# Kernel tuning notes

Measured on AMD Instinct MI355X. Metric: run time of the kernel, lower is better.

## Reference

```python
import jax, jax.numpy as jnp
import numpy as np

B, S, D, F, E, K, T = 4, 2048, 1024, 4096, 8, 2, 64


def setup_inputs() -> dict:
    key = jax.random.key(0)
    ks = jax.random.split(key, 12)
    s = 0.02
    return {
        "inputs": jax.random.normal(ks[0], (B, S, D), jnp.float32),
        "task_param": jax.random.normal(ks[1], (B, S, T), jnp.float32),
        "alpha": jnp.array(0.5, jnp.float32),
        "Wg_in": jax.random.normal(ks[2], (D, E), jnp.float32) * s,
        "bg_in": jnp.zeros((E,), jnp.float32),
        "Wg_task": jax.random.normal(ks[3], (T, E), jnp.float32) * s,
        "bg_task": jnp.zeros((E,), jnp.float32),
        "W1": jax.random.normal(ks[4], (E, D, F), jnp.float32) * s,
        "b1": jnp.zeros((E, F), jnp.float32),
        "W2": jax.random.normal(ks[5], (E, F, D), jnp.float32) * s,
        "b2": jnp.zeros((E, D), jnp.float32),
    }


def reference(inputs, task_param, alpha, Wg_in, bg_in, Wg_task, bg_task, W1, b1, W2, b2):
    dtype = inputs.dtype
    # blended gate logits: (1-alpha)*input_gate(x) + alpha*task_gate(task)
    gate_logits = (1.0 - alpha) * (jnp.einsum("bsd,de->bse", inputs, Wg_in) + bg_in) \
                + alpha * (jnp.einsum("bst,te->bse", task_param, Wg_task) + bg_task)
    # top-k expert selection (torch.topk: sorted descending)
    topk_vals, selected = jax.lax.top_k(gate_logits, K)  # [B,S,K]
    # aux load-balancing loss
    weights_softmax = jax.nn.softmax(gate_logits.astype(jnp.float32), axis=-1).astype(dtype)
    average_weight = weights_softmax.mean(axis=(0, 1))                 # [E]
    onehot = jax.nn.one_hot(selected, E, dtype=jnp.float32)            # [B,S,K,E]
    average_count = onehot.sum(axis=2).mean(axis=(0, 1)).astype(dtype) # [E]
    l_aux = jnp.mean(average_weight * average_count) * E
    # combine weights: softmax over the K selected logits, scattered to expert slots
    w = jax.nn.softmax(topk_vals.astype(jnp.float32), axis=-1).astype(dtype)  # [B,S,K]
    combine = jnp.einsum("bsk,bske->bse", w.astype(jnp.float32), onehot).astype(dtype)  # [B,S,E]
    # dense dispatch/combine (math-equivalent to boolean-mask gather/scatter loop)
    results = jnp.zeros_like(inputs)
    for e in range(E):
        h = jax.nn.gelu(jnp.einsum("bsd,df->bsf", inputs, W1[e]) + b1[e])
        y = jnp.einsum("bsf,fd->bsd", h, W2[e]) + b2[e]
        results = results + combine[..., e:e + 1] * y
    return (results, l_aux.astype(jnp.float32))
```

## Files before the change

### kernel.cpp

```cpp
#include <hip/hip_runtime.h>

#define NTOK 8192
#define DDIM 1024
#define FDIM 4096
#define NEXP 8
#define TDIM 64
#define MAXBLK 72

#define H_OFF   (1u<<20)
#define W1B_OFF (H_OFF + 134217728u)
#define W2B_OFF (W1B_OFF + 67108864u)
#define XB_OFF  (W2B_OFF + 67108864u)
#define FULL_WS (XB_OFF + 16777216u)

typedef __bf16 bf16x8 __attribute__((ext_vector_type(8)));
typedef unsigned short u16x8 __attribute__((ext_vector_type(8)));
typedef unsigned short u16x4 __attribute__((ext_vector_type(4)));
typedef float f32x4 __attribute__((ext_vector_type(4)));

__device__ __forceinline__ float gelu_tanh(float h) {
  float u = 0.7978845608028654f * (h + 0.044715f * h * h * h);
  float e = __expf(2.0f * u);
  return 0.5f * h * (2.0f - 2.0f / (e + 1.0f));
}

__device__ __forceinline__ void glds16(const void* g, void* l) {
  __builtin_amdgcn_global_load_lds((const __attribute__((address_space(1))) void*)g,
                                   (__attribute__((address_space(3))) void*)l, 16, 0, 0);
}

#define VM8() asm volatile("s_waitcnt vmcnt(8)" ::: "memory")
#define VM4() asm volatile("s_waitcnt vmcnt(4)" ::: "memory")
#define VM0() asm volatile("s_waitcnt vmcnt(0)" ::: "memory")
#define BAR() __builtin_amdgcn_s_barrier()

__global__ __launch_bounds__(256) void gate_kernel(
    const float* __restrict__ x, const float* __restrict__ task,
    const float* __restrict__ alpha_p,
    const float* __restrict__ Wg_in, const float* __restrict__ bg_in,
    const float* __restrict__ Wg_task, const float* __restrict__ bg_task,
    int* __restrict__ cnt, float* __restrict__ wsum,
    int* __restrict__ tok_list, float* __restrict__ wt_list)
{
  __shared__ float s_wsum[NEXP];
  int tid = threadIdx.x;
  if (tid < NEXP) s_wsum[tid] = 0.0f;
  __syncthreads();

  int lane = tid & 63;
  int wid  = tid >> 6;
  int tok  = blockIdx.x * 4 + wid;
  float a  = alpha_p[0];

  const float* xr = x + (size_t)tok * DDIM;
  float accd[8] = {0,0,0,0,0,0,0,0};
#pragma unroll
  for (int i = 0; i < DDIM/64; ++i) {
    int d = lane + 64*i;
    float xv = xr[d];
    f32x4 wa = *(const f32x4*)(Wg_in + (size_t)d*8);
    f32x4 wb = *(const f32x4*)(Wg_in + (size_t)d*8 + 4);
#pragma unroll
    for (int j = 0; j < 4; ++j) {
      accd[j]   = fmaf(xv, wa[j], accd[j]);
      accd[4+j] = fmaf(xv, wb[j], accd[4+j]);
    }
  }
  float part[8];
  {
    int d = lane;
    float tv = task[(size_t)tok*TDIM + d];
    f32x4 wa = *(const f32x4*)(Wg_task + (size_t)d*8);
    f32x4 wb = *(const f32x4*)(Wg_task + (size_t)d*8 + 4);
#pragma unroll
    for (int j = 0; j < 4; ++j) {
      part[j]   = (1.0f-a)*accd[j]   + a*(tv*wa[j]);
      part[4+j] = (1.0f-a)*accd[4+j] + a*(tv*wb[j]);
    }
  }
#pragma unroll
  for (int e = 0; e < 8; ++e) {
#pragma unroll
    for (int m = 1; m < 64; m <<= 1) part[e] += __shfl_xor(part[e], m);
  }

  if (lane == 0) {
    float lg[8];
#pragma unroll
    for (int e = 0; e < 8; ++e) lg[e] = part[e] + (1.0f-a)*bg_in[e] + a*bg_task[e];
    int e0 = 0;
#pragma unroll
    for (int e = 1; e < 8; ++e) if (lg[e] > lg[e0]) e0 = e;
    int e1 = (e0 == 0) ? 1 : 0;
#pragma unroll
    for (int e = 0; e < 8; ++e) if (e != e0 && lg[e] > lg[e1]) e1 = e;
    float mx = lg[0];
#pragma unroll
    for (int e = 1; e < 8; ++e) mx = fmaxf(mx, lg[e]);
    float p[8], s = 0.0f;
#pragma unroll
    for (int e = 0; e < 8; ++e) { p[e] = __expf(lg[e] - mx); s += p[e]; }
    float inv = 1.0f / s;
#pragma unroll
    for (int e = 0; e < 8; ++e) atomicAdd(&s_wsum[e], p[e] * inv);
    float p1 = __expf(lg[e1] - lg[e0]);
    float w0 = 1.0f / (1.0f + p1);
    float w1 = p1 * w0;
    int pos0 = atomicAdd(&cnt[e0], 1);
    tok_list[e0*NTOK + pos0] = tok; wt_list[e0*NTOK + pos0] = w0;
    int pos1 = atomicAdd(&cnt[e1], 1);
    tok_list[e1*NTOK + pos1] = tok; wt_list[e1*NTOK + pos1] = w1;
  }
  __syncthreads();
  if (tid < NEXP) atomicAdd(&wsum[tid], s_wsum[tid]);
}

__global__ void finalize_kernel(const int* __restrict__ cnt, const float* __restrict__ wsum,
                                int* __restrict__ offs, float* __restrict__ laux,
                                int* __restrict__ blk_e, int* __restrict__ blk_m)
{
  if (threadIdx.x == 0) {
    int o = 0; float l = 0.0f; int nb = 0;
    for (int e = 0; e < NEXP; ++e) {
      offs[e] = o;
      for (int m0 = 0; m0 < cnt[e]; m0 += 256) {
        if (nb < MAXBLK) { blk_e[nb] = e; blk_m[nb] = m0; ++nb; }
      }
      l += (wsum[e] * (1.0f/NTOK)) * ((float)cnt[e] * (1.0f/NTOK));
      o += cnt[e];
    }
    for (; nb < MAXBLK; ++nb) blk_e[nb] = -1;
    *laux = l;
  }
}

__global__ __launch_bounds__(256) void prep_x(const float* __restrict__ X,
                                              unsigned short* __restrict__ Xb)
{
  size_t i = ((size_t)blockIdx.x*256 + threadIdx.x)*8;
  f32x4 a = *(const f32x4*)(X + i);
  f32x4 b = *(const f32x4*)(X + i + 4);
  u16x8 v;
#pragma unroll
  for (int j = 0; j < 4; ++j) {
    v[j]   = __builtin_bit_cast(unsigned short, (__bf16)a[j]);
    v[4+j] = __builtin_bit_cast(unsigned short, (__bf16)b[j]);
  }
  *(u16x8*)(Xb + i) = v;
}

template<bool PERM>
__global__ __launch_bounds__(256) void prep_w(const float* __restrict__ W,
                                              unsigned short* __restrict__ Wb,
                                              int N, int NKB, int NJ)
{
  int kb = blockIdx.x, J = blockIdx.y, e = blockIdx.z;
  int K = NKB*64;
  __shared__ unsigned short t[64*264];
  int tid = threadIdx.x;
  const float* src = W + ((size_t)e*K + (size_t)kb*64) * N + J*256;
  int k = tid >> 2, cg = tid & 3;
#pragma unroll
  for (int ii = 0; ii < 16; ++ii) {
    int n = cg*64 + ii*4;
    f32x4 v = *(const f32x4*)(src + (size_t)k*N + n);
    u16x4 b;
#pragma unroll
    for (int j = 0; j < 4; ++j) b[j] = __builtin_bit_cast(unsigned short, (__bf16)v[j]);
    *(u16x4*)&t[k*264 + n] = b;
  }
  __syncthreads();
  unsigned short* dst = Wb + ((size_t)(e*NJ + J)*NKB + kb)*16384;
#pragma unroll
  for (int i = 0; i < 8; ++i) {
    int c2 = i*256 + tid;
    int cl = c2 & 1023;
    int h  = c2 >> 10;
    int R  = cl >> 3, dp = cl & 7;
    int d  = dp ^ (R & 7);
    int nloc = (R<<1) | (d>>2);
    int pbase = h*32 + (d&3)*8;
    u16x8 v;
#pragma unroll
    for (int j = 0; j < 8; ++j) {
      int v64 = pbase + j;
      int kl  = PERM ? (((v64 & 3) << 4) | (v64 >> 2)) : v64;
      v[j] = t[kl*264 + nloc];
    }
    *(u16x8*)(dst + (size_t)c2*8) = v;
  }
}


#define STAGE(bufbase, t) do {                                                \
  char* sa__ = ldsb + (bufbase);                                              \
  _Pragma("unroll")                                                           \
  for (int i_ = 0; i_ < 2; ++i_) {                                            \
    glds16(asrc[i_] + (size_t)(t)*64, sa__ + dstoff[i_]);                     \
    glds16(bsrc + (size_t)(t)*16384 + i_*8192, sa__ + 16384 + dstoff[i_]);    \
  }                                                                           \
} while (0)

#define COMPUTE(bufbase) do {                                                 \
  const unsigned short* sa_ = (const unsigned short*)(ldsb + (bufbase));      \
  const unsigned short* sb_ = sa_ + 8192;                                     \
  bf16x8 bfv_[4];                                                             \
  _Pragma("unroll")                                                           \
  for (int ni_ = 0; ni_ < 4; ++ni_)                                           \
    bfv_[ni_] = *(const bf16x8*)&sb_[boff0 + ni_*512];                        \
  __builtin_amdgcn_s_setprio(1);                                              \
  _Pragma("unroll")                                                           \
  for (int mi_ = 0; mi_ < 8; ++mi_) {                                         \
    bf16x8 af_ = *(const bf16x8*)&sa_[aoff0 + mi_*512];                       \
    _Pragma("unroll")                                                         \
    for (int ni_ = 0; ni_ < 4; ++ni_)                                         \
      acc[mi_][ni_] = __builtin_amdgcn_mfma_f32_16x16x32_bf16(af_, bfv_[ni_], acc[mi_][ni_], 0, 0, 0); \
  }                                                                           \
  __builtin_amdgcn_s_setprio(0);                                              \
} while (0)

__global__ __launch_bounds__(512) void gemm1_v5(
    const unsigned short* __restrict__ Xb, const unsigned short* __restrict__ W1b,
    const float* __restrict__ b1,
    const int* __restrict__ cnt, const int* __restrict__ offs,
    const int* __restrict__ tok_list,
    const int* __restrict__ blk_e, const int* __restrict__ blk_m,
    unsigned short* __restrict__ H)
{
  int e = blk_e[blockIdx.y];
  if (e < 0) return;
  int m0 = blk_m[blockIdx.y];
  int ce = cnt[e];
  int off = offs[e];
  int J = blockIdx.x;

  __shared__ __align__(16) char ldsb[131072];
  __shared__ int s_tok[256];

  int tid = threadIdx.x;
  if (tid < 256) {
    int idx = m0 + tid;
    s_tok[tid] = tok_list[e*NTOK + ((idx < ce) ? idx : (ce-1))];
  }
  __syncthreads();

  int l = tid & 63, w = tid >> 6;
  int wr = w >> 2, wc = w & 3;
  int q = l & 15, g = l >> 4;

  const char* asrc[2];
  int dstoff[2];
#pragma unroll
  for (int i = 0; i < 2; ++i) {
    int c = i*512 + tid;
    int R = c >> 3, dp = c & 7;
    int d = dp ^ (R & 7);
    int r = (R << 1) | (d >> 2);
    int kc = d & 3;
    asrc[i] = (const char*)(Xb + (size_t)s_tok[r]*DDIM) + kc*16;
    dstoff[i] = c*16;
  }
  const char* bsrc = (const char*)W1b + (size_t)((e*16 + J)*32) * 16384 + (size_t)tid*16;

  int rowA = wr*128 + q, rowB = wc*64 + q;
  int RA = rowA >> 1, RB = rowB >> 1;
  int dq = ((q & 1) << 2) | g;
  const int aoff0 = RA*64 + (dq ^ (RA & 7))*8;
  const int boff0 = RB*64 + (dq ^ (RB & 7))*8;

  f32x4 acc[8][4];
#pragma unroll
  for (int mi = 0; mi < 8; ++mi)
#pragma unroll
    for (int ni = 0; ni < 4; ++ni) acc[mi][ni] = (f32x4){0.f,0.f,0.f,0.f};

#define NT1 (DDIM/32)
  STAGE(0, 0); STAGE(32768, 1); STAGE(65536, 2);
  VM8(); BAR();
  for (int t = 0; t < NT1-3; ++t) {
    STAGE(((t+3)&3)*32768, t+3);
    COMPUTE((t&3)*32768);
    VM8(); BAR();
  }
  COMPUTE(((NT1-3)&3)*32768); VM4(); BAR();
  COMPUTE(((NT1-2)&3)*32768); VM0(); BAR();
  COMPUTE(((NT1-1)&3)*32768);

  int n0 = J*256;
  float bias[4];
#pragma unroll
  for (int ni = 0; ni < 4; ++ni) bias[ni] = b1[(size_t)e*FDIM + n0 + wc*64 + ni*16 + q];
#pragma unroll
  for (int mi = 0; mi < 8; ++mi) {
#pragma unroll
    for (int j = 0; j < 4; ++j) {
      int r = wr*128 + mi*16 + g*4 + j;
      if (m0 + r >= ce) continue;
      u16x4 hv;
#pragma unroll
      for (int ni = 0; ni < 4; ++ni) {
        float h = acc[mi][ni][j] + bias[ni];
        hv[ni] = __builtin_bit_cast(unsigned short, (__bf16)gelu_tanh(h));
      }
      *(u16x4*)&H[(size_t)(off + m0 + r)*FDIM + n0 + wc*64 + q*4] = hv;
    }
  }
}

__global__ __launch_bounds__(512) void gemm2_v5(
    const unsigned short* __restrict__ H, const unsigned short* __restrict__ W2b,
    const float* __restrict__ b2,
    const int* __restrict__ cnt, const int* __restrict__ offs,
    const int* __restrict__ tok_list, const float* __restrict__ wt_list,
    const int* __restrict__ blk_e, const int* __restrict__ blk_m,
    float* __restrict__ out)
{
  int e = blk_e[blockIdx.y];
  if (e < 0) return;
  int m0 = blk_m[blockIdx.y];
  int ce = cnt[e];
  int off = offs[e];
  int J = blockIdx.x;
  int s = blockIdx.z;

  __shared__ __align__(16) char ldsb[131072];
  __shared__ int   s_tok[256];
  __shared__ float s_wt[256];

  int tid = threadIdx.x;
  if (tid < 256) {
    int idx = m0 + tid;
    int cidx = (idx < ce) ? idx : (ce-1);
    s_tok[tid] = tok_list[e*NTOK + cidx];
    s_wt[tid]  = (idx < ce) ? wt_list[e*NTOK + cidx] : 0.0f;
  }
  __syncthreads();

  int l = tid & 63, w = tid >> 6;
  int wr = w >> 2, wc = w & 3;
  int q = l & 15, g = l >> 4;

  const char* asrc[2];
  int dstoff[2];
#pragma unroll
  for (int i = 0; i < 2; ++i) {
    int c = i*512 + tid;
    int R = c >> 3, dp = c & 7;
    int d = dp ^ (R & 7);
    int r = (R << 1) | (d >> 2);
    int kc = d & 3;
    int rr = (m0 + r < ce) ? r : (ce-1-m0);
    asrc[i] = (const char*)(H + (size_t)(off + m0 + rr)*FDIM) + kc*16 + s*4096;
    dstoff[i] = c*16;
  }
  const char* bsrc = (const char*)W2b + (size_t)((e*4 + J)*128 + s*64) * 16384 + (size_t)tid*16;

  int rowA = wr*128 + q, rowB = wc*64 + q;
  int RA = rowA >> 1, RB = rowB >> 1;
  int dq = ((q & 1) << 2) | g;
  const int aoff0 = RA*64 + (dq ^ (RA & 7))*8;
  const int boff0 = RB*64 + (dq ^ (RB & 7))*8;

  f32x4 acc[8][4];
#pragma unroll
  for (int mi = 0; mi < 8; ++mi)
#pragma unroll
    for (int ni = 0; ni < 4; ++ni) acc[mi][ni] = (f32x4){0.f,0.f,0.f,0.f};

#define NT2 (FDIM/32/2)
  STAGE(0, 0); STAGE(32768, 1); STAGE(65536, 2);
  VM8(); BAR();
  for (int t = 0; t < NT2-3; ++t) {
    STAGE(((t+3)&3)*32768, t+3);
    COMPUTE((t&3)*32768);
    VM8(); BAR();
  }
  COMPUTE(((NT2-3)&3)*32768); VM4(); BAR();
  COMPUTE(((NT2-2)&3)*32768); VM0(); BAR();
  COMPUTE(((NT2-1)&3)*32768);

  int n0 = J*256;
  float bias[4];
#pragma unroll
  for (int ni = 0; ni < 4; ++ni)
    bias[ni] = (s == 0) ? b2[(size_t)e*DDIM + n0 + wc*64 + ni*16 + q] : 0.0f;
#pragma unroll
  for (int mi = 0; mi < 8; ++mi) {
#pragma unroll
    for (int j = 0; j < 4; ++j) {
      int r = wr*128 + mi*16 + g*4 + j;
      if (m0 + r >= ce) continue;
      int tok = s_tok[r];
      float wt = s_wt[r];
      float* orow = out + (size_t)tok * DDIM;
#pragma unroll
      for (int ni = 0; ni < 4; ++ni) {
        float y = acc[mi][ni][j] + bias[ni];
        unsafeAtomicAdd(&orow[n0 + wc*64 + ni*16 + q], wt * y);
      }
    }
  }
}

extern "C" void kernel_launch(void* const* d_in, const int* in_sizes, int n_in,
                              void* d_out, int out_size, void* d_ws, size_t ws_size,
                              hipStream_t stream)
{
  const float* x       = (const float*)d_in[0];
  const float* task    = (const float*)d_in[1];
  const float* alpha   = (const float*)d_in[2];
  const float* Wg_in   = (const float*)d_in[3];
  const float* bg_in   = (const float*)d_in[4];
  const float* Wg_task = (const float*)d_in[5];
  const float* bg_task = (const float*)d_in[6];
  const float* W1      = (const float*)d_in[7];
  const float* b1      = (const float*)d_in[8];
  const float* W2      = (const float*)d_in[9];
  const float* b2      = (const float*)d_in[10];
  float* out = (float*)d_out;

  char* ws = (char*)d_ws;
  int*   cnt      = (int*)(ws + 0);
  float* wsum     = (float*)(ws + 32);
  int*   offs     = (int*)(ws + 64);
  int*   blk_e    = (int*)(ws + 128);
  int*   blk_m    = (int*)(ws + 512);
  int*   tok_list = (int*)(ws + 4096);
  float* wt_list  = (float*)(ws + 4096 + NTOK*NEXP*4);
  unsigned short* H   = (unsigned short*)(ws + H_OFF);
  unsigned short* W1b = (unsigned short*)(ws + W1B_OFF);
  unsigned short* W2b = (unsigned short*)(ws + W2B_OFF);
  unsigned short* Xb  = (unsigned short*)(ws + XB_OFF);

  hipMemsetAsync(d_out, 0, (size_t)out_size * sizeof(float), stream);
  hipMemsetAsync(ws, 0, 128, stream);
  gate_kernel<<<NTOK/4, 256, 0, stream>>>(x, task, alpha, Wg_in, bg_in, Wg_task, bg_task,
                                          cnt, wsum, tok_list, wt_list);
  finalize_kernel<<<1, 64, 0, stream>>>(cnt, wsum, offs, out + (size_t)NTOK*DDIM, blk_e, blk_m);
  prep_x<<<NTOK*DDIM/2048, 256, 0, stream>>>(x, Xb);
  prep_w<false><<<dim3(16, 16, NEXP), 256, 0, stream>>>(W1, W1b, FDIM, 16, 16);
  prep_w<true ><<<dim3(64,  4, NEXP), 256, 0, stream>>>(W2, W2b, DDIM, 64, 4);
  gemm1_v5<<<dim3(16, MAXBLK), 512, 0, stream>>>(Xb, W1b, b1, cnt, offs, tok_list,
                                                 blk_e, blk_m, H);
  gemm2_v5<<<dim3(4, MAXBLK, 2), 512, 0, stream>>>(H, W2b, b2, cnt, offs, tok_list, wt_list,
                                                   blk_e, blk_m, out);
}
```

Before: 911.6 us.

## Restructure GEMM K-loop into 4-phase ping-pong schedule with split A/B staging

Replaces the 4-buffer single-stage pipeline in both expert GEMMs with a double-buffered 64-wide K step split into four phases. Each phase handles half the M fragments and issues one A or B global-to-LDS load, with explicit barriers and a sched_barrier separating LDS reads from the MFMA cluster. The aim is to interleave memory issue with matrix work more finely and keep MFMA bursts uninterrupted. In exchange it adds two barriers per phase, which is more synchronization overhead per K step.

```diff
diff --git a/kernel.cpp b/kernel.cpp
--- a/kernel.cpp
+++ b/kernel.cpp
@@ -29,10 +29,8 @@
                                    (__attribute__((address_space(3))) void*)l, 16, 0, 0);
 }
 
-#define VM8() asm volatile("s_waitcnt vmcnt(8)" ::: "memory")
 #define VM4() asm volatile("s_waitcnt vmcnt(4)" ::: "memory")
 #define VM0() asm volatile("s_waitcnt vmcnt(0)" ::: "memory")
-#define BAR() __builtin_amdgcn_s_barrier()
 
 __global__ __launch_bounds__(256) void gate_kernel(
     const float* __restrict__ x, const float* __restrict__ task,
@@ -192,34 +190,66 @@
 }
 
 
-#define STAGE(bufbase, t) do {                                                \
-  char* sa__ = ldsb + (bufbase);                                              \
-  _Pragma("unroll")                                                           \
-  for (int i_ = 0; i_ < 2; ++i_) {                                            \
-    glds16(asrc[i_] + (size_t)(t)*64, sa__ + dstoff[i_]);                     \
-    glds16(bsrc + (size_t)(t)*16384 + i_*8192, sa__ + 16384 + dstoff[i_]);    \
-  }                                                                           \
+#define AG(b,kh) (ldsb + (((b)*2+(kh))<<14))
+#define BG(b,kh) (ldsb + 65536 + (((b)*2+(kh))<<14))
+
+#define STAGE_A(b,kh,gi) do { char* dA_ = AG(b,kh);                        \
+  glds16(asrc0 + (size_t)(gi)*64, dA_ + dstoff0);                          \
+  glds16(asrc1 + (size_t)(gi)*64, dA_ + dstoff1); } while (0)
+
+#define STAGE_B(b,kh,gi) do { char* dB_ = BG(b,kh);                        \
+  glds16(bsrc + (size_t)(gi)*16384,        dB_ + dstoff0);                 \
+  glds16(bsrc + (size_t)(gi)*16384 + 8192, dB_ + dstoff1); } while (0)
+
+#define PHASE(SA, SB, MIBASE, READB, STAGE_STMT, VM_STMT) do {              \
+  const unsigned short* sa_ = (const unsigned short*)(SA);                  \
+  bf16x8 af_[4];                                                            \
+  _Pragma("unroll")                                                         \
+  for (int i_ = 0; i_ < 4; ++i_)                                            \
+    af_[i_] = *(const bf16x8*)&sa_[aoff0 + (MIBASE + i_)*512];              \
+  if (READB) {                                                              \
+    const unsigned short* sb_ = (const unsigned short*)(SB);                \
+    _Pragma("unroll")                                                       \
+    for (int ni_ = 0; ni_ < 4; ++ni_)                                       \
+      bfv[ni_] = *(const bf16x8*)&sb_[boff0 + ni_*512];                     \
+  }                                                                         \
+  STAGE_STMT;                                                               \
+  VM_STMT;                                                                  \
+  __builtin_amdgcn_s_barrier();                                             \
+  asm volatile("s_waitcnt lgkmcnt(0)" ::: "memory");                        \
+  __builtin_amdgcn_sched_barrier(0);                                        \
+  __builtin_amdgcn_s_setprio(1);                                            \
+  _Pragma("unroll")                                                         \
+  for (int i_ = 0; i_ < 4; ++i_)                                            \
+    _Pragma("unroll")                                                       \
+    for (int ni_ = 0; ni_ < 4; ++ni_)                                       \
+      acc[MIBASE + i_][ni_] = __builtin_amdgcn_mfma_f32_16x16x32_bf16(      \
+          af_[i_], bfv[ni_], acc[MIBASE + i_][ni_], 0, 0, 0);               \
+  __builtin_amdgcn_s_setprio(0);                                            \
+  __builtin_amdgcn_s_barrier();                                             \
 } while (0)
 
-#define COMPUTE(bufbase) do {                                                 \
-  const unsigned short* sa_ = (const unsigned short*)(ldsb + (bufbase));      \
-  const unsigned short* sb_ = sa_ + 8192;                                     \
-  bf16x8 bfv_[4];                                                             \
-  _Pragma("unroll")                                                           \
-  for (int ni_ = 0; ni_ < 4; ++ni_)                                           \
-    bfv_[ni_] = *(const bf16x8*)&sb_[boff0 + ni_*512];                        \
-  __builtin_amdgcn_s_setprio(1);                                              \
-  _Pragma("unroll")                                                           \
-  for (int mi_ = 0; mi_ < 8; ++mi_) {                                         \
-    bf16x8 af_ = *(const bf16x8*)&sa_[aoff0 + mi_*512];                       \
-    _Pragma("unroll")                                                         \
-    for (int ni_ = 0; ni_ < 4; ++ni_)                                         \
-      acc[mi_][ni_] = __builtin_amdgcn_mfma_f32_16x16x32_bf16(af_, bfv_[ni_], acc[mi_][ni_], 0, 0, 0); \
-  }                                                                           \
-  __builtin_amdgcn_s_setprio(0);                                              \
+#define KLOOP(NT) do {                                                      \
+  STAGE_A(0,0,0); STAGE_B(0,0,0);                                           \
+  STAGE_A(0,1,1); STAGE_B(0,1,1);                                           \
+  STAGE_A(1,0,2); STAGE_B(1,0,2);                                           \
+  VM4();                                                                    \
+  __builtin_amdgcn_s_barrier();                                             \
+  int b_ = 0;                                                               \
+  for (int t_ = 0; t_ < (NT); ++t_, b_ ^= 1) {                              \
+    PHASE(AG(b_,0), BG(b_,0), 0, 1,                                         \
+          { if (t_+1 < (NT)) STAGE_A(b_^1, 1, 2*(t_+1)+1); }, {});          \
+    PHASE(AG(b_,0), BG(b_,0), 4, 0,                                         \
+          { if (t_+1 < (NT)) STAGE_B(b_^1, 1, 2*(t_+1)+1); }, {});          \
+    PHASE(AG(b_,1), BG(b_,1), 0, 1,                                         \
+          { if (t_+2 < (NT)) STAGE_A(b_, 0, 2*(t_+2)); }, {});              \
+    PHASE(AG(b_,1), BG(b_,1), 4, 0,                                         \
+          { if (t_+2 < (NT)) STAGE_B(b_, 0, 2*(t_+2)); },                   \
+          { if (t_+2 < (NT)) VM4(); else VM0(); });                         \
+  }                                                                         \
 } while (0)
 
-__global__ __launch_bounds__(512) void gemm1_v5(
+__global__ __launch_bounds__(512) void gemm1_v6(
     const unsigned short* __restrict__ Xb, const unsigned short* __restrict__ W1b,
     const float* __restrict__ b1,
     const int* __restrict__ cnt, const int* __restrict__ offs,
@@ -248,22 +278,17 @@
   int wr = w >> 2, wc = w & 3;
   int q = l & 15, g = l >> 4;
 
-  const char* asrc[2];
-  int dstoff[2];
-#pragma unroll
-  for (int i = 0; i < 2; ++i) {
-    int c = i*512 + tid;
-    int R = c >> 3, dp = c & 7;
-    int d = dp ^ (R & 7);
-    int r = (R << 1) | (d >> 2);
-    int kc = d & 3;
-    asrc[i] = (const char*)(Xb + (size_t)s_tok[r]*DDIM) + kc*16;
-    dstoff[i] = c*16;
-  }
+  const char* asrc0; const char* asrc1;
+  {
+    int c0 = tid,        R0 = c0 >> 3, d0 = (c0 & 7) ^ (R0 & 7);
+    int c1 = 512 + tid,  R1 = c1 >> 3, d1 = (c1 & 7) ^ (R1 & 7);
+    asrc0 = (const char*)(Xb + (size_t)s_tok[(R0<<1)|(d0>>2)]*DDIM) + (d0 & 3)*16;
+    asrc1 = (const char*)(Xb + (size_t)s_tok[(R1<<1)|(d1>>2)]*DDIM) + (d1 & 3)*16;
+  }
+  const int dstoff0 = tid*16, dstoff1 = tid*16 + 8192;
   const char* bsrc = (const char*)W1b + (size_t)((e*16 + J)*32) * 16384 + (size_t)tid*16;
 
-  int rowA = wr*128 + q, rowB = wc*64 + q;
-  int RA = rowA >> 1, RB = rowB >> 1;
+  int RA = (wr*128 + q) >> 1, RB = (wc*64 + q) >> 1;
   int dq = ((q & 1) << 2) | g;
   const int aoff0 = RA*64 + (dq ^ (RA & 7))*8;
   const int boff0 = RB*64 + (dq ^ (RB & 7))*8;
@@ -273,18 +298,9 @@
   for (int mi = 0; mi < 8; ++mi)
 #pragma unroll
     for (int ni = 0; ni < 4; ++ni) acc[mi][ni] = (f32x4){0.f,0.f,0.f,0.f};
-
-#define NT1 (DDIM/32)
-  STAGE(0, 0); STAGE(32768, 1); STAGE(65536, 2);
-  VM8(); BAR();
-  for (int t = 0; t < NT1-3; ++t) {
-    STAGE(((t+3)&3)*32768, t+3);
-    COMPUTE((t&3)*32768);
-    VM8(); BAR();
-  }
-  COMPUTE(((NT1-3)&3)*32768); VM4(); BAR();
-  COMPUTE(((NT1-2)&3)*32768); VM0(); BAR();
-  COMPUTE(((NT1-1)&3)*32768);
+  bf16x8 bfv[4];
+
+  KLOOP(DDIM/64);
 
   int n0 = J*256;
   float bias[4];
@@ -307,7 +323,7 @@
   }
 }
 
-__global__ __launch_bounds__(512) void gemm2_v5(
+__global__ __launch_bounds__(512) void gemm2_v6(
     const unsigned short* __restrict__ H, const unsigned short* __restrict__ W2b,
     const float* __restrict__ b2,
     const int* __restrict__ cnt, const int* __restrict__ offs,
@@ -340,23 +356,20 @@
   int wr = w >> 2, wc = w & 3;
   int q = l & 15, g = l >> 4;
 
-  const char* asrc[2];
-  int dstoff[2];
-#pragma unroll
-  for (int i = 0; i < 2; ++i) {
-    int c = i*512 + tid;
-    int R = c >> 3, dp = c & 7;
-    int d = dp ^ (R & 7);
-    int r = (R << 1) | (d >> 2);
-    int kc = d & 3;
-    int rr = (m0 + r < ce) ? r : (ce-1-m0);
-    asrc[i] = (const char*)(H + (size_t)(off + m0 + rr)*FDIM) + kc*16 + s*4096;
-    dstoff[i] = c*16;
-  }
+  const char* asrc0; const char* asrc1;
+  {
+    int c0 = tid,        R0 = c0 >> 3, d0 = (c0 & 7) ^ (R0 & 7);
+    int c1 = 512 + tid,  R1 = c1 >> 3, d1 = (c1 & 7) ^ (R1 & 7);
+    int r0 = (R0<<1)|(d0>>2), r1 = (R1<<1)|(d1>>2);
+    int rr0 = (m0 + r0 < ce) ? r0 : (ce-1-m0);
+    int rr1 = (m0 + r1 < ce) ? r1 : (ce-1-m0);
+    asrc0 = (const char*)(H + (size_t)(off + m0 + rr0)*FDIM) + (d0 & 3)*16 + s*4096;
+    asrc1 = (const char*)(H + (size_t)(off + m0 + rr1)*FDIM) + (d1 & 3)*16 + s*4096;
+  }
+  const int dstoff0 = tid*16, dstoff1 = tid*16 + 8192;
   const char* bsrc = (const char*)W2b + (size_t)((e*4 + J)*128 + s*64) * 16384 + (size_t)tid*16;
 
-  int rowA = wr*128 + q, rowB = wc*64 + q;
-  int RA = rowA >> 1, RB = rowB >> 1;
+  int RA = (wr*128 + q) >> 1, RB = (wc*64 + q) >> 1;
   int dq = ((q & 1) << 2) | g;
   const int aoff0 = RA*64 + (dq ^ (RA & 7))*8;
   const int boff0 = RB*64 + (dq ^ (RB & 7))*8;
@@ -366,18 +379,9 @@
   for (int mi = 0; mi < 8; ++mi)
 #pragma unroll
     for (int ni = 0; ni < 4; ++ni) acc[mi][ni] = (f32x4){0.f,0.f,0.f,0.f};
-
-#define NT2 (FDIM/32/2)
-  STAGE(0, 0); STAGE(32768, 1); STAGE(65536, 2);
-  VM8(); BAR();
-  for (int t = 0; t < NT2-3; ++t) {
-    STAGE(((t+3)&3)*32768, t+3);
-    COMPUTE((t&3)*32768);
-    VM8(); BAR();
-  }
-  COMPUTE(((NT2-3)&3)*32768); VM4(); BAR();
-  COMPUTE(((NT2-2)&3)*32768); VM0(); BAR();
-  COMPUTE(((NT2-1)&3)*32768);
+  bf16x8 bfv[4];
+
+  KLOOP(FDIM/64/2);
 
   int n0 = J*256;
   float bias[4];
@@ -440,8 +444,8 @@
   prep_x<<<NTOK*DDIM/2048, 256, 0, stream>>>(x, Xb);
   prep_w<false><<<dim3(16, 16, NEXP), 256, 0, stream>>>(W1, W1b, FDIM, 16, 16);
   prep_w<true ><<<dim3(64,  4, NEXP), 256, 0, stream>>>(W2, W2b, DDIM, 64, 4);
-  gemm1_v5<<<dim3(16, MAXBLK), 512, 0, stream>>>(Xb, W1b, b1, cnt, offs, tok_list,
+  gemm1_v6<<<dim3(16, MAXBLK), 512, 0, stream>>>(Xb, W1b, b1, cnt, offs, tok_list,
                                                  blk_e, blk_m, H);
-  gemm2_v5<<<dim3(4, MAXBLK, 2), 512, 0, stream>>>(H, W2b, b2, cnt, offs, tok_list, wt_list,
+  gemm2_v6<<<dim3(4, MAXBLK, 2), 512, 0, stream>>>(H, W2b, b2, cnt, offs, tok_list, wt_list,
                                                    blk_e, blk_m, out);
 }
```

Result: faster. 856.0 us (-6.1%).
